# Optimization experiments

Measured on AMD Instinct MI355X. Metric: run time of the kernel, lower is better.

Reference implementation:

```python
import jax, jax.numpy as jnp
import numpy as np

N = 20000      # cells (nodes)
E = 640000     # kNN edges (before self loops)
IN = 2000      # gene features
C = 64         # out_channels
H = 4          # attention heads
NEG_SLOPE = 0.2
EPS = 1e-12


def setup_inputs() -> dict:
    key = jax.random.key(0)
    ks = jax.random.split(key, 12)
    s = lambda k, shape, sc: (jax.random.normal(k, shape, jnp.float32) * sc)
    x = s(ks[0], (N, IN), 1.0)
    edge_index = jax.random.randint(ks[1], (2, E), 0, N)
    W_ae = s(ks[2], (IN, C), 0.02); b_ae = jnp.zeros((C,), jnp.float32)
    Wl = s(ks[3], (C, H * C), 0.1); bl = jnp.zeros((H * C,), jnp.float32)
    Wr = s(ks[4], (C, H * C), 0.1); br = jnp.zeros((H * C,), jnp.float32)
    att = s(ks[5], (H, C), 0.1)
    b_conv = jnp.zeros((H * C,), jnp.float32)
    W_lin = s(ks[6], (H * C, C), 0.1); b_lin = jnp.zeros((C,), jnp.float32)
    ln_w = jnp.ones((C,), jnp.float32); ln_b = jnp.zeros((C,), jnp.float32)
    return dict(x=x, edge_index=edge_index, W_ae=W_ae, b_ae=b_ae, Wl=Wl, bl=bl,
                Wr=Wr, br=br, att=att, b_conv=b_conv, W_lin=W_lin, b_lin=b_lin,
                ln_w=ln_w, ln_b=ln_b)


def reference(x, edge_index, W_ae, b_ae, Wl, bl, Wr, br, att, b_conv,
              W_lin, b_lin, ln_w, ln_b):
    # Encoder.AE: linear projection of gene features -> node embeddings
    h = x @ W_ae + b_ae                              # [N, C]

    # GATv2Conv (PyG defaults: add_self_loops=True, negative_slope=0.2,
    # dropout is identity at eval, concat=True)
    loops = jnp.arange(N)
    src = jnp.concatenate([edge_index[0], loops])    # [E+N] message sources j
    dst = jnp.concatenate([edge_index[1], loops])    # [E+N] targets i

    xl = (h @ Wl + bl).reshape(N, H, C)              # W_l x (source features)
    xr = (h @ Wr + br).reshape(N, H, C)              # W_r x (target features)

    g = jax.nn.leaky_relu(xl[src] + xr[dst], NEG_SLOPE)   # [E+N, H, C]
    logits = jnp.einsum('ehc,hc->eh', g, att)             # [E+N, H]

    # segment softmax over incoming edges of each target node
    m = jax.ops.segment_max(logits, dst, num_segments=N)  # [N, H]
    e = jnp.exp(logits - m[dst])
    denom = jax.ops.segment_sum(e, dst, num_segments=N)   # [N, H] (>0: self loops)
    alpha = e / denom[dst]                                 # [E+N, H]

    out = jax.ops.segment_sum(alpha[:, :, None] * xl[src], dst, num_segments=N)
    out = out.reshape(N, H * C) + b_conv             # concat heads + bias

    # Encoder.linear + activation (relu), dropout = identity at eval
    a = jax.nn.relu(out @ W_lin + b_lin)             # [N, C]

    # residual + TF-style LayerNorm
    y = a + h
    u = y.mean(-1, keepdims=True)
    v = ((y - u) ** 2).mean(-1, keepdims=True)
    return ln_w * (y - u) / jnp.sqrt(v + EPS) + ln_b
```

## Files before the change

kernel.cpp:

```cpp
#include <hip/hip_runtime.h>
#include <hip/hip_fp16.h>

#define N_NODES 20000
#define N_EDGES 640000
#define IN_F    2000
#define KPAD    2048
#define C_OUT   64
#define HC      256
#define NEG     0.2f
#define SCAN_B  79

typedef __attribute__((ext_vector_type(4))) float f32x4;
typedef __attribute__((ext_vector_type(8))) short bf16x8;
typedef _Float16 h2 __attribute__((ext_vector_type(2)));
typedef _Float16 f16x8 __attribute__((ext_vector_type(8)));

__device__ inline unsigned short f2bf(float f) {
    unsigned u = __float_as_uint(f);
    return (unsigned short)((u + 0x7FFFu + ((u >> 16) & 1u)) >> 16);
}

__device__ inline unsigned cvt_pk_bf16(float lo, float hi) {
    unsigned r;
    asm("v_cvt_pk_bf16_f32 %0, %1, %2" : "=v"(r) : "v"(lo), "v"(hi));
    return r;
}


__global__ void k_hist(const int* __restrict__ dst, int* __restrict__ counts) {
    int e = blockIdx.x * blockDim.x + threadIdx.x;
    if (e < N_EDGES) atomicAdd(&counts[dst[e]], 1);
}

__global__ void k_scan1(const int* __restrict__ counts, int* __restrict__ bsum) {
    int t = threadIdx.x, b = blockIdx.x;
    int i = b * 256 + t;
    int v = (i < N_NODES) ? counts[i] : 0;
    int s = v;
    #pragma unroll
    for (int d = 1; d < 64; d <<= 1) s += __shfl_xor(s, d, 64);
    __shared__ int ws[4];
    if ((t & 63) == 0) ws[t >> 6] = s;
    __syncthreads();
    if (t == 0) bsum[b] = ws[0] + ws[1] + ws[2] + ws[3];
}

__global__ void k_scan2(const int* __restrict__ bsum, int* __restrict__ bbase,
                        int* __restrict__ offsets) {
    int lane = threadIdx.x;
    int v0 = (lane < SCAN_B) ? bsum[lane] : 0;
    int v1 = (64 + lane < SCAN_B) ? bsum[64 + lane] : 0;
    int s0 = v0;
    #pragma unroll
    for (int d = 1; d < 64; d <<= 1) { int t = __shfl_up(s0, d, 64); if (lane >= d) s0 += t; }
    int tot0 = __shfl(s0, 63, 64);
    int s1 = v1;
    #pragma unroll
    for (int d = 1; d < 64; d <<= 1) { int t = __shfl_up(s1, d, 64); if (lane >= d) s1 += t; }
    int tot1 = __shfl(s1, 63, 64);
    if (lane < SCAN_B) bbase[lane] = s0 - v0;
    if (64 + lane < SCAN_B) bbase[64 + lane] = tot0 + s1 - v1;
    if (lane == 0) offsets[N_NODES] = tot0 + tot1;
}

__global__ void k_scan3(const int* __restrict__ counts, const int* __restrict__ bbase,
                        int* __restrict__ offsets, int* __restrict__ cursor) {
    int t = threadIdx.x, b = blockIdx.x;
    int lane = t & 63, wid = t >> 6;
    int i = b * 256 + t;
    int v = (i < N_NODES) ? counts[i] : 0;
    int s = v;
    #pragma unroll
    for (int d = 1; d < 64; d <<= 1) { int u = __shfl_up(s, d, 64); if (lane >= d) s += u; }
    __shared__ int ws[4];
    if (lane == 63) ws[wid] = s;
    __syncthreads();
    int wb = 0;
    #pragma unroll
    for (int w = 0; w < 3; ++w) if (w < wid) wb += ws[w];
    int excl = bbase[b] + wb + (s - v);
    if (i < N_NODES) { offsets[i] = excl; cursor[i] = excl; }
}

__global__ void k_scatter(const int* __restrict__ src, const int* __restrict__ dst,
                          int* __restrict__ cursor, int* __restrict__ ssrc) {
    int e = blockIdx.x * blockDim.x + threadIdx.x;
    if (e < N_EDGES) {
        int d = dst[e];
        int p = atomicAdd(&cursor[d], 1);
        ssrc[p] = src[e];
    }
}


__global__ void k_wt(const float* __restrict__ W, unsigned short* __restrict__ Wpk) {
    int idx = blockIdx.x * 256 + threadIdx.x;
    int n = idx >> 11;
    int k = idx & 2047;
    float v = (k < IN_F) ? W[(size_t)k * C_OUT + n] : 0.f;
    Wpk[(size_t)(k >> 3) * 512 + n * 8 + (k & 7)] = f2bf(v);
}

__global__ void k_wlin16(const float* __restrict__ W, unsigned short* __restrict__ Wt16) {
    int idx = blockIdx.x * 256 + threadIdx.x;
    int col = idx >> 8;
    int k = idx & 255;
    _Float16 v = (_Float16)W[(size_t)k * C_OUT + col];
    Wt16[(size_t)col * HC + k] = __builtin_bit_cast(unsigned short, v);
}


__global__ __launch_bounds__(512) void k_gemm_h(
    const float* __restrict__ x, const unsigned short* __restrict__ Wpk,
    const float* __restrict__ b, float* __restrict__ h) {
    __shared__ float red[16][7][64];
    int t = threadIdx.x;
    int lane = t & 63, w = t >> 6;
    int row0 = blockIdx.x * 16;
    int r = lane & 15, kc = lane >> 4;
    const float* xrow = x + (size_t)(row0 + r) * IN_F;
    f32x4 acc[4] = {{0,0,0,0},{0,0,0,0},{0,0,0,0},{0,0,0,0}};

    int kstart = w * 256;
    #pragma unroll
    for (int s = 0; s < 8; ++s) {
        int kb = kstart + s * 32 + kc * 8;
        int kbc = kb <= 1992 ? kb : 1992;
        float4 f0 = *(const float4*)&xrow[kbc];
        float4 f1 = *(const float4*)&xrow[kbc + 4];
        uint4 uu;
        uu.x = cvt_pk_bf16(f0.x, f0.y);
        uu.y = cvt_pk_bf16(f0.z, f0.w);
        uu.z = cvt_pk_bf16(f1.x, f1.y);
        uu.w = cvt_pk_bf16(f1.z, f1.w);
        if (kb > 1992) { uu.x = 0u; uu.y = 0u; uu.z = 0u; uu.w = 0u; }
        bf16x8 af = __builtin_bit_cast(bf16x8, uu);
        const unsigned short* bp = Wpk + (size_t)(kb >> 3) * 512;
        #pragma unroll
        for (int cb = 0; cb < 4; ++cb) {
            bf16x8 bf = *(const bf16x8*)&bp[(cb * 16 + r) * 8];
            acc[cb] = __builtin_amdgcn_mfma_f32_16x16x32_bf16(af, bf, acc[cb], 0, 0, 0);
        }
    }

    if (w > 0) {
        #pragma unroll
        for (int cb = 0; cb < 4; ++cb)
            #pragma unroll
            for (int rr = 0; rr < 4; ++rr)
                red[cb * 4 + rr][w - 1][lane] = acc[cb][rr];
    }
    __syncthreads();
    if (w == 0) {
        #pragma unroll
        for (int cb = 0; cb < 4; ++cb)
            #pragma unroll
            for (int rr = 0; rr < 4; ++rr) {
                float s = acc[cb][rr];
                #pragma unroll
                for (int ww = 0; ww < 7; ++ww)
                    s += red[cb * 4 + rr][ww][lane];
                acc[cb][rr] = s;
            }
        int ci = kc * 4, cj = r;
        #pragma unroll
        for (int cb = 0; cb < 4; ++cb) {
            int col = cb * 16 + cj;
            float bb = b[col];
            #pragma unroll
            for (int rr = 0; rr < 4; ++rr)
                h[(size_t)(row0 + ci + rr) * C_OUT + col] = acc[cb][rr] + bb;
        }
    }
}


__global__ __launch_bounds__(256) void k_xlxr2(
    const float* __restrict__ h, const float* __restrict__ Wl, const float* __restrict__ bl,
    const float* __restrict__ Wr, const float* __restrict__ br,
    unsigned short* __restrict__ xlh, float* __restrict__ xr) {
    __shared__ float hs[64][68];
    __shared__ float Ws[64][128];
    int t = threadIdx.x;
    int mb = blockIdx.x >> 2, nb = blockIdx.x & 3;
    int node0 = mb * 64;
    const float* Wsrc = (nb < 2) ? (Wl + nb * 128) : (Wr + (nb - 2) * 128);
    const float* bsrc = (nb < 2) ? (bl + nb * 128) : (br + (nb - 2) * 128);

    {
        int row = t >> 2, q = t & 3;
        int gnode = node0 + row; if (gnode >= N_NODES) gnode = N_NODES - 1;
        const float4* src = (const float4*)&h[(size_t)gnode * C_OUT + q * 16];
        *(float4*)&hs[row][q * 16 + 0]  = src[0];
        *(float4*)&hs[row][q * 16 + 4]  = src[1];
        *(float4*)&hs[row][q * 16 + 8]  = src[2];
        *(float4*)&hs[row][q * 16 + 12] = src[3];
    }
    {
        #pragma unroll
        for (int i = 0; i < 8; ++i) {
            int f = t + i * 256;
            int k = f >> 5, c4 = (f & 31) << 2;
            *(float4*)&Ws[k][c4] = *(const float4*)&Wsrc[(size_t)k * HC + c4];
        }
    }
    __syncthreads();

    int tr = t >> 5;
    int tc = t & 31;
    float4 acc[8];
    float4 bv = *(const float4*)&bsrc[tc * 4];
    #pragma unroll
    for (int r = 0; r < 8; ++r) acc[r] = bv;

    for (int k4 = 0; k4 < 64; k4 += 4) {
        float4 w0 = *(float4*)&Ws[k4 + 0][tc * 4];
        float4 w1 = *(float4*)&Ws[k4 + 1][tc * 4];
        float4 w2 = *(float4*)&Ws[k4 + 2][tc * 4];
        float4 w3 = *(float4*)&Ws[k4 + 3][tc * 4];
        #pragma unroll
        for (int r = 0; r < 8; ++r) {
            float4 a = *(float4*)&hs[tr * 8 + r][k4];
            acc[r].x += a.x * w0.x + a.y * w1.x + a.z * w2.x + a.w * w3.x;
            acc[r].y += a.x * w0.y + a.y * w1.y + a.z * w2.y + a.w * w3.y;
            acc[r].z += a.x * w0.z + a.y * w1.z + a.z * w2.z + a.w * w3.z;
            acc[r].w += a.x * w0.w + a.y * w1.w + a.z * w2.w + a.w * w3.w;
        }
    }
    #pragma unroll
    for (int r = 0; r < 8; ++r) {
        int gnode = node0 + tr * 8 + r;
        if (gnode < N_NODES) {
            if (nb < 2) {
                h2 lo = { (_Float16)acc[r].x, (_Float16)acc[r].y };
                h2 hi = { (_Float16)acc[r].z, (_Float16)acc[r].w };
                uint2 o = { __builtin_bit_cast(unsigned, lo),
                            __builtin_bit_cast(unsigned, hi) };
                *(uint2*)&xlh[(size_t)gnode * HC + nb * 128 + tc * 4] = o;
            } else {
                *(float4*)&xr[(size_t)gnode * HC + (nb - 2) * 128 + tc * 4] = acc[r];
            }
        }
    }
}


__global__ __launch_bounds__(256) void k_attn(
    const unsigned short* __restrict__ xlh, const float* __restrict__ xr,
    const int* __restrict__ offsets, const int* __restrict__ ssrc,
    const float* __restrict__ att, const float* __restrict__ b_conv,
    unsigned short* __restrict__ ovh) {
    int wid = threadIdx.x >> 6, lane = threadIdx.x & 63;
    int node = blockIdx.x * 4 + wid;
    int sub = lane >> 4;
    int sl  = lane & 15;
    int c0  = sl * 16;

    const h2 z2  = { (_Float16)0.f, (_Float16)0.f };
    const h2 ns2 = { (_Float16)NEG, (_Float16)NEG };

    h2 xr2[8], at2[8];
    #pragma unroll
    for (int i = 0; i < 4; ++i) {
        float4 t4 = *(const float4*)&xr[(size_t)node * HC + c0 + i * 4];
        xr2[i*2+0] = h2{ (_Float16)t4.x, (_Float16)t4.y };
        xr2[i*2+1] = h2{ (_Float16)t4.z, (_Float16)t4.w };
        float4 a4 = *(const float4*)&att[c0 + i * 4];
        at2[i*2+0] = h2{ (_Float16)a4.x, (_Float16)a4.y };
        at2[i*2+1] = h2{ (_Float16)a4.z, (_Float16)a4.w };
    }
    h2 acc2[8];
    #pragma unroll
    for (int i = 0; i < 8; ++i) acc2[i] = z2;
    float denom = 0.f;

    auto load_edge = [&](int j, uint4& w0, uint4& w1) {
        const uint4* rp = (const uint4*)&xlh[(size_t)j * HC + c0];
        w0 = rp[0]; w1 = rp[1];
    };
    auto compute_edge = [&](uint4 w0, uint4 w1, bool valid) {
        h2 x2[8];
        x2[0] = __builtin_bit_cast(h2, w0.x); x2[1] = __builtin_bit_cast(h2, w0.y);
        x2[2] = __builtin_bit_cast(h2, w0.z); x2[3] = __builtin_bit_cast(h2, w0.w);
        x2[4] = __builtin_bit_cast(h2, w1.x); x2[5] = __builtin_bit_cast(h2, w1.y);
        x2[6] = __builtin_bit_cast(h2, w1.z); x2[7] = __builtin_bit_cast(h2, w1.w);
        h2 p2 = z2;
        #pragma unroll
        for (int i = 0; i < 8; ++i) {
            h2 g  = x2[i] + xr2[i];
            h2 gs = g * ns2;
            g = __builtin_elementwise_max(g, gs);
            p2 += g * at2[i];
        }
        float p = (float)p2.x + (float)p2.y;
        p += __shfl_xor(p, 1); p += __shfl_xor(p, 2);
        float ex = valid ? __expf(p) : 0.f;
        denom += ex;
        h2 e2 = { (_Float16)ex, (_Float16)ex };
        #pragma unroll
        for (int i = 0; i < 8; ++i) acc2[i] += e2 * x2[i];
    };

    {
        uint4 s0v, s1v;
        load_edge(node, s0v, s1v);
        compute_edge(s0v, s1v, sub == 0);
    }

    int s0 = offsets[node], s1 = offsets[node + 1];
    for (int base = s0; base < s1; base += 64) {
        int rem = s1 - base;
        int cnt = rem < 64 ? rem : 64;
        int jv = (base + lane < s1) ? ssrc[base + lane] : 0;
        int niter = (cnt + 3) >> 2;
        uint4 a0, a1, b0, b1;
        int jA = __shfl(jv, sub, 64);
        load_edge(jA, a0, a1);
        for (int it = 0; it < niter; it += 2) {
            int eB = ((it + 1) << 2) + sub;
            int jB = __shfl(jv, eB & 63, 64);
            load_edge(jB, b0, b1);
            compute_edge(a0, a1, ((it << 2) + sub) < cnt);
            int eA2 = ((it + 2) << 2) + sub;
            int jA2 = __shfl(jv, eA2 & 63, 64);
            load_edge(jA2, a0, a1);
            compute_edge(b0, b1, eB < cnt);
        }
    }

    float accf[16];
    #pragma unroll
    for (int i = 0; i < 8; ++i) {
        accf[2*i]   = (float)acc2[i].x;
        accf[2*i+1] = (float)acc2[i].y;
    }
    #pragma unroll
    for (int i = 0; i < 16; ++i) {
        accf[i] += __shfl_xor(accf[i], 16);
        accf[i] += __shfl_xor(accf[i], 32);
    }
    denom += __shfl_xor(denom, 16);
    denom += __shfl_xor(denom, 32);

    float inv = 1.f / denom;
    if (sub == 0) {
        float bcf[16];
        #pragma unroll
        for (int i = 0; i < 4; ++i) {
            float4 bc = *(const float4*)&b_conv[c0 + i * 4];
            bcf[i*4+0] = bc.x; bcf[i*4+1] = bc.y; bcf[i*4+2] = bc.z; bcf[i*4+3] = bc.w;
        }
        unsigned ww[8];
        #pragma unroll
        for (int i = 0; i < 8; ++i) {
            h2 p = { (_Float16)(accf[2*i]   * inv + bcf[2*i]),
                     (_Float16)(accf[2*i+1] * inv + bcf[2*i+1]) };
            ww[i] = __builtin_bit_cast(unsigned, p);
        }
        uint4 o0 = { ww[0], ww[1], ww[2], ww[3] };
        uint4 o1 = { ww[4], ww[5], ww[6], ww[7] };
        *(uint4*)&ovh[(size_t)node * HC + c0]     = o0;
        *(uint4*)&ovh[(size_t)node * HC + c0 + 8] = o1;
    }
}


__global__ __launch_bounds__(256) void k_post(
    const unsigned short* __restrict__ ovh, const unsigned short* __restrict__ Wt16,
    const float* __restrict__ b_lin, const float* __restrict__ hbuf,
    const float* __restrict__ ln_w, const float* __restrict__ ln_b,
    float* __restrict__ out) {
    int t = threadIdx.x;
    int lane = t & 63, w = t >> 6;
    int node0 = blockIdx.x * 64 + w * 16;
    int r = lane & 15, kc = lane >> 4;
    int noder = node0 + r;
    int nodec = noder < N_NODES ? noder : N_NODES - 1;

    f32x4 acc[4] = {{0,0,0,0},{0,0,0,0},{0,0,0,0},{0,0,0,0}};
    #pragma unroll
    for (int k0 = 0; k0 < HC; k0 += 32) {
        int kb = k0 + kc * 8;
        f16x8 af = *(const f16x8*)&ovh[(size_t)nodec * HC + kb];
        #pragma unroll
        for (int cb = 0; cb < 4; ++cb) {
            f16x8 bf = *(const f16x8*)&Wt16[(size_t)(cb * 16 + r) * HC + kb];
            acc[cb] = __builtin_amdgcn_mfma_f32_16x16x32_f16(af, bf, acc[cb], 0, 0, 0);
        }
    }

    int ci = (lane >> 4) * 4, cj = lane & 15;
    #pragma unroll
    for (int rr = 0; rr < 4; ++rr) {
        int grow = node0 + ci + rr;
        int growc = grow < N_NODES ? grow : N_NODES - 1;
        float y[4];
        float ssum = 0.f;
        #pragma unroll
        for (int cb = 0; cb < 4; ++cb) {
            int col = cb * 16 + cj;
            float a = acc[cb][rr] + b_lin[col];
            a = a > 0.f ? a : 0.f;
            float yy = a + hbuf[(size_t)growc * C_OUT + col];
            y[cb] = yy;
            ssum += yy;
        }
        ssum += __shfl_xor(ssum, 1); ssum += __shfl_xor(ssum, 2);
        ssum += __shfl_xor(ssum, 4); ssum += __shfl_xor(ssum, 8);
        float m = ssum * (1.f / 64.f);
        float vs = 0.f;
        #pragma unroll
        for (int cb = 0; cb < 4; ++cb) { float d = y[cb] - m; vs += d * d; }
        vs += __shfl_xor(vs, 1); vs += __shfl_xor(vs, 2);
        vs += __shfl_xor(vs, 4); vs += __shfl_xor(vs, 8);
        float rinv = rsqrtf(vs * (1.f / 64.f) + 1e-12f);
        if (grow < N_NODES) {
            #pragma unroll
            for (int cb = 0; cb < 4; ++cb) {
                int col = cb * 16 + cj;
                out[(size_t)grow * C_OUT + col] =
                    ln_w[col] * (y[cb] - m) * rinv + ln_b[col];
            }
        }
    }
}


extern "C" void kernel_launch(void* const* d_in, const int* in_sizes, int n_in,
                              void* d_out, int out_size, void* d_ws, size_t ws_size,
                              hipStream_t stream) {
    const float* x     = (const float*)d_in[0];
    const int*   ei    = (const int*)  d_in[1];
    const float* W_ae  = (const float*)d_in[2];
    const float* b_ae  = (const float*)d_in[3];
    const float* Wl    = (const float*)d_in[4];
    const float* bl    = (const float*)d_in[5];
    const float* Wr    = (const float*)d_in[6];
    const float* br    = (const float*)d_in[7];
    const float* att   = (const float*)d_in[8];
    const float* b_conv= (const float*)d_in[9];
    const float* W_lin = (const float*)d_in[10];
    const float* b_lin = (const float*)d_in[11];
    const float* ln_w  = (const float*)d_in[12];
    const float* ln_b  = (const float*)d_in[13];
    float* out = (float*)d_out;
    const int* src = ei;
    const int* dst = ei + N_EDGES;

    char* ws = (char*)d_ws;
    size_t off = 0;
    auto alloc = [&](size_t bytes) {
        void* p = ws + off;
        off = (off + bytes + 255) & ~(size_t)255;
        return p;
    };
    float* h       = (float*)alloc((size_t)N_NODES * C_OUT * 4);
    unsigned short* xlh = (unsigned short*)alloc((size_t)N_NODES * HC * 2);
    float* xr      = (float*)alloc((size_t)N_NODES * HC * 4);
    unsigned short* ovh = (unsigned short*)alloc((size_t)N_NODES * HC * 2);
    int*   counts  = (int*)  alloc((size_t)N_NODES * 4);
    int*   offsets = (int*)  alloc((size_t)(N_NODES + 1) * 4);
    int*   cursor  = (int*)  alloc((size_t)N_NODES * 4);
    int*   ssrc    = (int*)  alloc((size_t)N_EDGES * 4);
    unsigned short* Wpk  = (unsigned short*)alloc((size_t)C_OUT * KPAD * 2);
    unsigned short* Wt16 = (unsigned short*)alloc((size_t)C_OUT * HC * 2);
    int*   bsum    = (int*)  alloc((size_t)SCAN_B * 4);
    int*   bbase   = (int*)  alloc((size_t)SCAN_B * 4);

    (void)hipMemsetAsync(counts, 0, (size_t)N_NODES * 4, stream);
    k_hist   <<<(N_EDGES + 255) / 256, 256, 0, stream>>>(dst, counts);
    k_scan1  <<<SCAN_B, 256, 0, stream>>>(counts, bsum);
    k_scan2  <<<1, 64, 0, stream>>>(bsum, bbase, offsets);
    k_scan3  <<<SCAN_B, 256, 0, stream>>>(counts, bbase, offsets, cursor);
    k_scatter<<<(N_EDGES + 255) / 256, 256, 0, stream>>>(src, dst, cursor, ssrc);
    k_wt     <<<(C_OUT * KPAD) / 256, 256, 0, stream>>>(W_ae, Wpk);
    k_wlin16 <<<(C_OUT * HC) / 256, 256, 0, stream>>>(W_lin, Wt16);
    k_gemm_h <<<N_NODES / 16, 512, 0, stream>>>(x, Wpk, b_ae, h);
    k_xlxr2  <<<((N_NODES + 63) / 64) * 4, 256, 0, stream>>>(h, Wl, bl, Wr, br, xlh, xr);
    k_attn   <<<N_NODES / 4, 256, 0, stream>>>(xlh, xr, offsets, ssrc, att, b_conv, ovh);
    k_post   <<<(N_NODES + 63) / 64, 256, 0, stream>>>(ovh, Wt16, b_lin, h,
                                                       ln_w, ln_b, out);
}
```

Measured before the change: 195.0 us.

## Store xl head-major and split attention across heads via grid y

The fp16 source features are now written head-major ([H][N][64]) instead of node-major, and the attention kernel launches one block column per head. Each wave processes one node and one head, with 8 lanes per edge covering 64 channels and 8 edges in flight. The aim is a smaller per-head gather working set for better cache locality and more parallelism across blocks. In exchange, offsets, indices and xr are read four times, and each edge gather is only 128 bytes.

```diff
diff --git a/kernel.cpp b/kernel.cpp
--- a/kernel.cpp
+++ b/kernel.cpp
@@ -178,7 +178,7 @@
 __global__ __launch_bounds__(256) void k_xlxr2(
     const float* __restrict__ h, const float* __restrict__ Wl, const float* __restrict__ bl,
     const float* __restrict__ Wr, const float* __restrict__ br,
-    unsigned short* __restrict__ xlh, float* __restrict__ xr) {
+    unsigned short* __restrict__ xlhm, float* __restrict__ xr) {
     __shared__ float hs[64][68];
     __shared__ float Ws[64][128];
     int t = threadIdx.x;
@@ -232,11 +232,14 @@
         int gnode = node0 + tr * 8 + r;
         if (gnode < N_NODES) {
             if (nb < 2) {
+                int col  = nb * 128 + tc * 4;
+                int head = col >> 6;
+                int chin = col & 63;
                 h2 lo = { (_Float16)acc[r].x, (_Float16)acc[r].y };
                 h2 hi = { (_Float16)acc[r].z, (_Float16)acc[r].w };
                 uint2 o = { __builtin_bit_cast(unsigned, lo),
                             __builtin_bit_cast(unsigned, hi) };
-                *(uint2*)&xlh[(size_t)gnode * HC + nb * 128 + tc * 4] = o;
+                *(uint2*)&xlhm[((size_t)head * N_NODES + gnode) * 64 + chin] = o;
             } else {
                 *(float4*)&xr[(size_t)gnode * HC + (nb - 2) * 128 + tc * 4] = acc[r];
             }
@@ -246,65 +249,64 @@
 
 
 __global__ __launch_bounds__(256) void k_attn(
-    const unsigned short* __restrict__ xlh, const float* __restrict__ xr,
+    const unsigned short* __restrict__ xlhm, const float* __restrict__ xr,
     const int* __restrict__ offsets, const int* __restrict__ ssrc,
     const float* __restrict__ att, const float* __restrict__ b_conv,
     unsigned short* __restrict__ ovh) {
     int wid = threadIdx.x >> 6, lane = threadIdx.x & 63;
     int node = blockIdx.x * 4 + wid;
-    int sub = lane >> 4;
-    int sl  = lane & 15;
-    int c0  = sl * 16;
+    int head = blockIdx.y;
+    int sub = lane >> 3;
+    int sl  = lane & 7;
+    int cg  = head * 64 + sl * 8;
+    const unsigned short* xbase = xlhm + (size_t)head * N_NODES * 64 + sl * 8;
 
     const h2 z2  = { (_Float16)0.f, (_Float16)0.f };
     const h2 ns2 = { (_Float16)NEG, (_Float16)NEG };
 
-    h2 xr2[8], at2[8];
-    #pragma unroll
-    for (int i = 0; i < 4; ++i) {
-        float4 t4 = *(const float4*)&xr[(size_t)node * HC + c0 + i * 4];
+    h2 xr2[4], at2[4];
+    #pragma unroll
+    for (int i = 0; i < 2; ++i) {
+        float4 t4 = *(const float4*)&xr[(size_t)node * HC + cg + i * 4];
         xr2[i*2+0] = h2{ (_Float16)t4.x, (_Float16)t4.y };
         xr2[i*2+1] = h2{ (_Float16)t4.z, (_Float16)t4.w };
-        float4 a4 = *(const float4*)&att[c0 + i * 4];
+        float4 a4 = *(const float4*)&att[cg + i * 4];
         at2[i*2+0] = h2{ (_Float16)a4.x, (_Float16)a4.y };
         at2[i*2+1] = h2{ (_Float16)a4.z, (_Float16)a4.w };
     }
-    h2 acc2[8];
-    #pragma unroll
-    for (int i = 0; i < 8; ++i) acc2[i] = z2;
+    h2 acc2[4];
+    #pragma unroll
+    for (int i = 0; i < 4; ++i) acc2[i] = z2;
     float denom = 0.f;
 
-    auto load_edge = [&](int j, uint4& w0, uint4& w1) {
-        const uint4* rp = (const uint4*)&xlh[(size_t)j * HC + c0];
-        w0 = rp[0]; w1 = rp[1];
+    auto load_edge = [&](int j, uint4& w0) {
+        w0 = *(const uint4*)&xbase[(size_t)j * 64];
     };
-    auto compute_edge = [&](uint4 w0, uint4 w1, bool valid) {
-        h2 x2[8];
+    auto compute_edge = [&](uint4 w0, bool valid) {
+        h2 x2[4];
         x2[0] = __builtin_bit_cast(h2, w0.x); x2[1] = __builtin_bit_cast(h2, w0.y);
         x2[2] = __builtin_bit_cast(h2, w0.z); x2[3] = __builtin_bit_cast(h2, w0.w);
-        x2[4] = __builtin_bit_cast(h2, w1.x); x2[5] = __builtin_bit_cast(h2, w1.y);
-        x2[6] = __builtin_bit_cast(h2, w1.z); x2[7] = __builtin_bit_cast(h2, w1.w);
         h2 p2 = z2;
         #pragma unroll
-        for (int i = 0; i < 8; ++i) {
+        for (int i = 0; i < 4; ++i) {
             h2 g  = x2[i] + xr2[i];
             h2 gs = g * ns2;
             g = __builtin_elementwise_max(g, gs);
             p2 += g * at2[i];
         }
         float p = (float)p2.x + (float)p2.y;
-        p += __shfl_xor(p, 1); p += __shfl_xor(p, 2);
+        p += __shfl_xor(p, 1); p += __shfl_xor(p, 2); p += __shfl_xor(p, 4);
         float ex = valid ? __expf(p) : 0.f;
         denom += ex;
         h2 e2 = { (_Float16)ex, (_Float16)ex };
         #pragma unroll
-        for (int i = 0; i < 8; ++i) acc2[i] += e2 * x2[i];
+        for (int i = 0; i < 4; ++i) acc2[i] += e2 * x2[i];
     };
 
     {
-        uint4 s0v, s1v;
-        load_edge(node, s0v, s1v);
-        compute_edge(s0v, s1v, sub == 0);
+        uint4 s0v;
+        load_edge(node, s0v);
+        compute_edge(s0v, sub == 0);
     }
 
     int s0 = offsets[node], s1 = offsets[node + 1];
@@ -312,55 +314,55 @@
         int rem = s1 - base;
         int cnt = rem < 64 ? rem : 64;
         int jv = (base + lane < s1) ? ssrc[base + lane] : 0;
-        int niter = (cnt + 3) >> 2;
-        uint4 a0, a1, b0, b1;
+        int niter = (cnt + 7) >> 3;
+        uint4 a0, b0;
         int jA = __shfl(jv, sub, 64);
-        load_edge(jA, a0, a1);
+        load_edge(jA, a0);
         for (int it = 0; it < niter; it += 2) {
-            int eB = ((it + 1) << 2) + sub;
+            int eB = ((it + 1) << 3) + sub;
             int jB = __shfl(jv, eB & 63, 64);
-            load_edge(jB, b0, b1);
-            compute_edge(a0, a1, ((it << 2) + sub) < cnt);
-            int eA2 = ((it + 2) << 2) + sub;
+            load_edge(jB, b0);
+            compute_edge(a0, ((it << 3) + sub) < cnt);
+            int eA2 = ((it + 2) << 3) + sub;
             int jA2 = __shfl(jv, eA2 & 63, 64);
-            load_edge(jA2, a0, a1);
-            compute_edge(b0, b1, eB < cnt);
-        }
-    }
-
-    float accf[16];
-    #pragma unroll
-    for (int i = 0; i < 8; ++i) {
+            load_edge(jA2, a0);
+            compute_edge(b0, eB < cnt);
+        }
+    }
+
+    float accf[8];
+    #pragma unroll
+    for (int i = 0; i < 4; ++i) {
         accf[2*i]   = (float)acc2[i].x;
         accf[2*i+1] = (float)acc2[i].y;
     }
     #pragma unroll
-    for (int i = 0; i < 16; ++i) {
+    for (int i = 0; i < 8; ++i) {
+        accf[i] += __shfl_xor(accf[i], 8);
         accf[i] += __shfl_xor(accf[i], 16);
         accf[i] += __shfl_xor(accf[i], 32);
     }
+    denom += __shfl_xor(denom, 8);
     denom += __shfl_xor(denom, 16);
     denom += __shfl_xor(denom, 32);
 
     float inv = 1.f / denom;
     if (sub == 0) {
-        float bcf[16];
+        float bcf[8];
+        #pragma unroll
+        for (int i = 0; i < 2; ++i) {
+            float4 bc = *(const float4*)&b_conv[cg + i * 4];
+            bcf[i*4+0] = bc.x; bcf[i*4+1] = bc.y; bcf[i*4+2] = bc.z; bcf[i*4+3] = bc.w;
+        }
+        unsigned ww[4];
         #pragma unroll
         for (int i = 0; i < 4; ++i) {
-            float4 bc = *(const float4*)&b_conv[c0 + i * 4];
-            bcf[i*4+0] = bc.x; bcf[i*4+1] = bc.y; bcf[i*4+2] = bc.z; bcf[i*4+3] = bc.w;
-        }
-        unsigned ww[8];
-        #pragma unroll
-        for (int i = 0; i < 8; ++i) {
             h2 p = { (_Float16)(accf[2*i]   * inv + bcf[2*i]),
                      (_Float16)(accf[2*i+1] * inv + bcf[2*i+1]) };
             ww[i] = __builtin_bit_cast(unsigned, p);
         }
         uint4 o0 = { ww[0], ww[1], ww[2], ww[3] };
-        uint4 o1 = { ww[4], ww[5], ww[6], ww[7] };
-        *(uint4*)&ovh[(size_t)node * HC + c0]     = o0;
-        *(uint4*)&ovh[(size_t)node * HC + c0 + 8] = o1;
+        *(uint4*)&ovh[(size_t)node * HC + cg] = o0;
     }
 }
 
@@ -455,7 +457,7 @@
         return p;
     };
     float* h       = (float*)alloc((size_t)N_NODES * C_OUT * 4);
-    unsigned short* xlh = (unsigned short*)alloc((size_t)N_NODES * HC * 2);
+    unsigned short* xlhm = (unsigned short*)alloc((size_t)N_NODES * HC * 2);
     float* xr      = (float*)alloc((size_t)N_NODES * HC * 4);
     unsigned short* ovh = (unsigned short*)alloc((size_t)N_NODES * HC * 2);
     int*   counts  = (int*)  alloc((size_t)N_NODES * 4);
@@ -476,8 +478,9 @@
     k_wt     <<<(C_OUT * KPAD) / 256, 256, 0, stream>>>(W_ae, Wpk);
     k_wlin16 <<<(C_OUT * HC) / 256, 256, 0, stream>>>(W_lin, Wt16);
     k_gemm_h <<<N_NODES / 16, 512, 0, stream>>>(x, Wpk, b_ae, h);
-    k_xlxr2  <<<((N_NODES + 63) / 64) * 4, 256, 0, stream>>>(h, Wl, bl, Wr, br, xlh, xr);
-    k_attn   <<<N_NODES / 4, 256, 0, stream>>>(xlh, xr, offsets, ssrc, att, b_conv, ovh);
+    k_xlxr2  <<<((N_NODES + 63) / 64) * 4, 256, 0, stream>>>(h, Wl, bl, Wr, br, xlhm, xr);
+    k_attn   <<<dim3(N_NODES / 4, 4), 256, 0, stream>>>(xlhm, xr, offsets, ssrc,
+                                                        att, b_conv, ovh);
     k_post   <<<(N_NODES + 63) / 64, 256, 0, stream>>>(ovh, Wt16, b_lin, h,
                                                        ln_w, ln_b, out);
 }
```

Result: slower. 207.4 us (+6.3%).
